# Optimization experiments

Hardware: AMD Instinct MI355X
Metric: run time of the kernel (lower is better)

The kernel has to match this reference:

```python
import jax, jax.numpy as jnp
import numpy as np

D_MODEL = 256
N_HEADS = 8
HEAD_DIM = D_MODEL // N_HEADS  # 32
N_LEVELS = 4
N_POINTS = 4
LEVEL_SHAPES = [(100, 100), (50, 50), (25, 25), (13, 13)]
LEVEL_STARTS = [0] + list(np.cumsum([h * w for h, w in LEVEL_SHAPES]))[:-1]
LEN_IN = int(sum(h * w for h, w in LEVEL_SHAPES))  # 13294
BATCH = 2
LEN_Q = LEN_IN  # encoder self-attention


def _offset_bias():
    # faithful to MSDeformAttn._reset_parameters for sampling_offsets bias
    thetas = np.arange(N_HEADS, dtype=np.float32) * (2.0 * np.pi / N_HEADS)
    grid = np.stack([np.cos(thetas), np.sin(thetas)], -1)
    grid = grid / np.abs(grid).max(-1, keepdims=True)
    grid = np.tile(grid.reshape(N_HEADS, 1, 1, 2), (1, N_LEVELS, N_POINTS, 1))
    for i in range(N_POINTS):
        grid[:, :, i, :] *= i + 1
    return jnp.asarray(grid.reshape(-1), dtype=jnp.float32)


def setup_inputs() -> dict:
    key = jax.random.key(0)
    ks = jax.random.split(key, 10)
    s = 1.0 / np.sqrt(D_MODEL)
    inp = {
        "query": jax.random.normal(ks[0], (BATCH, LEN_Q, D_MODEL), jnp.float32),
        "reference_points": jax.random.uniform(ks[1], (BATCH, LEN_Q, N_LEVELS, 2), jnp.float32),
        "input_flatten": jax.random.normal(ks[2], (BATCH, LEN_IN, D_MODEL), jnp.float32),
        "input_spatial_shapes": jnp.asarray(LEVEL_SHAPES, dtype=jnp.int32),
        "W_value": jax.random.normal(ks[3], (D_MODEL, D_MODEL), jnp.float32) * s,
        "b_value": jnp.zeros((D_MODEL,), jnp.float32),
        "W_off": jax.random.normal(ks[4], (D_MODEL, N_HEADS * N_LEVELS * N_POINTS * 2), jnp.float32) * 0.01,
        "b_off": _offset_bias(),
        "W_attn": jax.random.normal(ks[5], (D_MODEL, N_HEADS * N_LEVELS * N_POINTS), jnp.float32) * 0.01,
        "b_attn": jnp.zeros((N_HEADS * N_LEVELS * N_POINTS,), jnp.float32),
        "W_out": jax.random.normal(ks[6], (D_MODEL, D_MODEL), jnp.float32) * s,
        "b_out": jnp.zeros((D_MODEL,), jnp.float32),
    }
    return inp


def _corner(v_t, ix, iy, h, w):
    # v_t: (n, M, h*w, D); ix/iy: (n, M, LqP) int32. Zero padding outside.
    valid = (ix >= 0) & (ix < w) & (iy >= 0) & (iy < h)
    idx = jnp.clip(iy, 0, h - 1) * w + jnp.clip(ix, 0, w - 1)
    g = jnp.take_along_axis(v_t, idx[..., None], axis=2)  # (n, M, LqP, D)
    return g * valid[..., None].astype(v_t.dtype)


def _ms_deform_attn(query, reference_points, input_flatten,
                    W_value, b_value, W_off, b_off, W_attn, b_attn, W_out, b_out):
    n, lq, _ = query.shape
    value = (input_flatten @ W_value + b_value).reshape(n, LEN_IN, N_HEADS, HEAD_DIM)
    offs = (query @ W_off + b_off).reshape(n, lq, N_HEADS, N_LEVELS, N_POINTS, 2)
    aw = jax.nn.softmax(
        (query @ W_attn + b_attn).reshape(n, lq, N_HEADS, N_LEVELS * N_POINTS), axis=-1
    ).reshape(n, lq, N_HEADS, N_LEVELS, N_POINTS)
    # offset_normalizer = (w, h) per level
    norm = jnp.asarray([[w, h] for h, w in LEVEL_SHAPES], dtype=query.dtype)
    loc = reference_points[:, :, None, :, None, :] + offs / norm[None, None, None, :, None, :]

    acc = jnp.zeros((n, N_HEADS, lq, HEAD_DIM), dtype=value.dtype)
    for l, (h, w) in enumerate(LEVEL_SHAPES):
        s0 = LEVEL_STARTS[l]
        v_t = jnp.transpose(value[:, s0:s0 + h * w], (0, 2, 1, 3))  # (n, M, hw, D)
        ll = loc[:, :, :, l]  # (n, lq, M, P, 2) in [0,1]
        # grid_sample bilinear, align_corners=False: pixel = coord*size - 0.5
        x = ll[..., 0] * w - 0.5
        y = ll[..., 1] * h - 0.5
        x0 = jnp.floor(x); y0 = jnp.floor(y)
        tx = x - x0; ty = y - y0
        ix0 = x0.astype(jnp.int32); iy0 = y0.astype(jnp.int32)
        flat = lambda a: jnp.transpose(a, (0, 2, 1, 3)).reshape(n, N_HEADS, lq * N_POINTS)
        ix0f, iy0f = flat(ix0), flat(iy0)
        txf = flat(tx)[..., None]; tyf = flat(ty)[..., None]
        g00 = _corner(v_t, ix0f, iy0f, h, w)
        g01 = _corner(v_t, ix0f + 1, iy0f, h, w)
        g10 = _corner(v_t, ix0f, iy0f + 1, h, w)
        g11 = _corner(v_t, ix0f + 1, iy0f + 1, h, w)
        samp = (g00 * (1 - txf) * (1 - tyf) + g01 * txf * (1 - tyf)
                + g10 * (1 - txf) * tyf + g11 * txf * tyf)
        samp = samp.reshape(n, N_HEADS, lq, N_POINTS, HEAD_DIM)
        wl = jnp.transpose(aw[:, :, :, l], (0, 2, 1, 3))[..., None]  # (n, M, lq, P, 1)
        acc = acc + (samp * wl).sum(axis=3)

    out = jnp.transpose(acc, (0, 2, 1, 3)).reshape(n, lq, D_MODEL)
    return out @ W_out + b_out


def reference(query, reference_points, input_flatten, input_spatial_shapes,
              W_value, b_value, W_off, b_off, W_attn, b_attn, W_out, b_out):
    # input_spatial_shapes carried for signature fidelity; level geometry is static.
    return _ms_deform_attn(query, reference_points, input_flatten,
                           W_value, b_value, W_off, b_off, W_attn, b_attn, W_out, b_out)
```

## Files before the change

### kernel.cpp

```cpp
#include <hip/hip_runtime.h>

#define NH 8
#define HD 32
#define NL 4
#define NP 4
#define DM 256
#define LEN_IN_C 13294
#define LQ_C 13294
#define B_C 2
#define M_TOTAL (B_C * LQ_C)
#define MT_TILES 1662
#define RT32_TILES 831
#define GQ 32
#define QBLKS 831

typedef __attribute__((ext_vector_type(8))) short short8;
typedef __attribute__((ext_vector_type(4))) float floatx4;
typedef __attribute__((ext_vector_type(2))) float floatx2;

__device__ __forceinline__ unsigned short f2bf(float x) {
    union { float f; unsigned int u; } a; a.f = x;
    unsigned int r = (a.u + 0x7FFFu + ((a.u >> 16) & 1u)) >> 16;
    return (unsigned short)r;
}
__device__ __forceinline__ floatx2 up2(unsigned int u) {
    union { unsigned int u; float f; } lo, hi;
    lo.u = u << 16; hi.u = u & 0xffff0000u;
    floatx2 r; r.x = lo.f; r.y = hi.f; return r;
}
__device__ __forceinline__ unsigned int cvtpk_bf16(float lo, float hi) {
    unsigned int r;
    asm("v_cvt_pk_bf16_f32 %0, %1, %2" : "=v"(r) : "v"(lo), "v"(hi));
    return r;
}

__device__ __forceinline__ void conv_b_body(const float* __restrict__ W,
                                            unsigned short* __restrict__ Bsw,
                                            int Nsrc, int NTsrc, int NTtotal, int ntOff,
                                            int vblk) {
    const int u = vblk * 256 + threadIdx.x;
    const int lane = u & 63;
    const int unit = u >> 6;
    const int ntl = unit % NTsrc;
    const int kc = unit / NTsrc;
    const int n = ntl * 16 + (lane & 15);
    const int k0 = kc * 32 + (lane >> 4) * 8;
    short8 v;
#pragma unroll
    for (int j = 0; j < 8; ++j)
        v[j] = (short)f2bf(W[(size_t)(k0 + j) * Nsrc + n]);
    ((short8*)Bsw)[(size_t)(kc * NTtotal + ntOff + ntl) * 64 + lane] = v;
}

__global__ __launch_bounds__(256) void conv_weights_kernel(const float* __restrict__ Wv,
                                                           const float* __restrict__ Woff,
                                                           const float* __restrict__ Wattn,
                                                           const float* __restrict__ Wout,
                                                           const float* __restrict__ boff,
                                                           const float* __restrict__ battn,
                                                           unsigned short* __restrict__ BswV,
                                                           unsigned short* __restrict__ BswOA,
                                                           unsigned short* __restrict__ BswO,
                                                           float* __restrict__ fbias,
                                                           unsigned short* __restrict__ value,
                                                           unsigned short* __restrict__ AccSw) {
    const int blk = blockIdx.x;
    if (blk < 32)        conv_b_body(Wv,    BswV,  256, 16, 16, 0,  blk);
    else if (blk < 64)   conv_b_body(Woff,  BswOA, 256, 16, 24, 0,  blk - 32);
    else if (blk < 80)   conv_b_body(Wattn, BswOA, 128,  8, 24, 16, blk - 64);
    else if (blk < 112)  conv_b_body(Wout,  BswO,  256, 16, 16, 0,  blk - 80);
    else if (blk < 114) {
        const int t = (blk - 112) * 256 + threadIdx.x;
        if (t < 384) fbias[t] = (t < 256) ? boff[t] : battn[t - 256];
        else if (t < 416) {
            const int j = t - 384;
            value[-32 + j] = 0;
            value[(size_t)M_TOTAL * 256 + j] = 0;
        }
    } else {
        const int idx = threadIdx.x;
        if (idx < 128) {
            const int kc = idx >> 4;
            const int sub = idx & 15;
            const int lane = (12 + (sub & 3)) + 16 * (sub >> 2);
            const size_t unit = (size_t)(1661 * 8 + kc) * 64 + lane;
            short8 z = (short8){0, 0, 0, 0, 0, 0, 0, 0};
            ((short8*)AccSw)[unit] = z;
        }
    }
}

template <int NT, int OUTMODE>
__device__ __forceinline__ void gemm_lds_full(unsigned short* __restrict__ sA,
                                              const float* __restrict__ A,
                                              const unsigned short* __restrict__ Bsw,
                                              const float* __restrict__ bias,
                                              void* __restrict__ Cout, int M, int rt32) {
    constexpr int NTW = NT / 4;
    const int tid = threadIdx.x;
    const int lane = tid & 63;
    const int wave = tid >> 6;
    const int trow = rt32 * 32;

#pragma unroll
    for (int i = 0; i < 8; ++i) {
        const int li = i * 1024 + tid * 4;
        const int lrow = li >> 8;
        const int lcol = li & 255;
        const int srow = min(trow + lrow, M - 1);
        const float4 f = *(const float4*)(A + (size_t)srow * 256 + lcol);
        uint2 pk;
        pk.x = cvtpk_bf16(f.x, f.y);
        pk.y = cvtpk_bf16(f.z, f.w);
        const int lb = (li * 2) ^ ((lrow & 7) << 4);
        *(uint2*)((char*)sA + lb) = pk;
    }
    __syncthreads();

    const int m = lane & 15;
    const int q = lane >> 4;
    const short8* Bu = (const short8*)Bsw;

    floatx4 acc[2][NTW];
#pragma unroll
    for (int r = 0; r < 2; ++r)
#pragma unroll
        for (int t = 0; t < NTW; ++t) acc[r][t] = (floatx4){0.f, 0.f, 0.f, 0.f};

    const int swz = (m & 7) << 4;
#pragma unroll 2
    for (int kc = 0; kc < 8; ++kc) {
        const int fb0 = (m * 512 + kc * 64 + q * 16) ^ swz;
        const int fb1 = ((m + 16) * 512 + kc * 64 + q * 16) ^ swz;
        const short8 a0 = *(const short8*)((const char*)sA + fb0);
        const short8 a1 = *(const short8*)((const char*)sA + fb1);
#pragma unroll
        for (int t = 0; t < NTW; ++t) {
            const short8 b = Bu[(size_t)(kc * NT + wave * NTW + t) * 64 + lane];
            acc[0][t] = __builtin_amdgcn_mfma_f32_16x16x32_bf16(a0, b, acc[0][t], 0, 0, 0);
            acc[1][t] = __builtin_amdgcn_mfma_f32_16x16x32_bf16(a1, b, acc[1][t], 0, 0, 0);
        }
    }

    const int N = NT * 16;
    const int colq = lane & 15;
    const int rowq = (lane >> 4) * 4;
#pragma unroll
    for (int t = 0; t < NTW; ++t) {
        const int col = (wave * NTW + t) * 16 + colq;
        const float bc = bias[col];
#pragma unroll
        for (int r = 0; r < 2; ++r) {
#pragma unroll
            for (int reg = 0; reg < 4; ++reg) {
                const int row = trow + r * 16 + rowq + reg;
                if (row < M) {
                    const float v = acc[r][t][reg] + bc;
                    if (OUTMODE == 1) {
                        const int bb = row >= LEN_IN_C;
                        const int pos = row - (bb ? LEN_IN_C : 0);
                        const int hh = col >> 5;
                        const int dd = col & 31;
                        ((unsigned short*)Cout)[((size_t)((bb << 3) + hh) * LEN_IN_C + pos) * 32 + dd] = f2bf(v);
                    } else {
                        ((float*)Cout)[(size_t)row * N + col] = v;
                    }
                }
            }
        }
    }
}

__global__ __launch_bounds__(256) void front_gemm_kernel(const float* __restrict__ inflat,
                                                         const float* __restrict__ query,
                                                         const unsigned short* __restrict__ BswV,
                                                         const unsigned short* __restrict__ BswOA,
                                                         const float* __restrict__ bv,
                                                         const float* __restrict__ fbias,
                                                         unsigned short* __restrict__ value,
                                                         float* __restrict__ fused, int M) {
    __shared__ unsigned short sA[32 * 256];
    const int x = blockIdx.x;
    const int rt32 = x >> 1;
    if ((x & 1) == 0)
        gemm_lds_full<16, 1>(sA, inflat, BswV, bv, (void*)value, M, rt32);
    else
        gemm_lds_full<24, 0>(sA, query, BswOA, fbias, (void*)fused, M, rt32);
}

__global__ __launch_bounds__(256) void back_gemm_kernel(const unsigned short* __restrict__ Asw,
                                                        const unsigned short* __restrict__ Bsw,
                                                        const float* __restrict__ bias,
                                                        float* __restrict__ Cout, int M) {
    constexpr int NT = 16;
    constexpr int NTW = 4;
    const int tid = threadIdx.x;
    const int lane = tid & 63;
    const int wave = tid >> 6;
    const int rt = blockIdx.x;

    const short8* Au = (const short8*)Asw;
    const short8* Bu = (const short8*)Bsw;

    floatx4 acc[NTW];
#pragma unroll
    for (int t = 0; t < NTW; ++t) acc[t] = (floatx4){0.f, 0.f, 0.f, 0.f};

#pragma unroll 2
    for (int kc = 0; kc < 8; ++kc) {
        const short8 a = Au[(size_t)(rt * 8 + kc) * 64 + lane];
#pragma unroll
        for (int t = 0; t < NTW; ++t) {
            const short8 b = Bu[(size_t)(kc * NT + wave * NTW + t) * 64 + lane];
            acc[t] = __builtin_amdgcn_mfma_f32_16x16x32_bf16(a, b, acc[t], 0, 0, 0);
        }
    }

    const int colq = lane & 15;
    const int rowq = (lane >> 4) * 4;
#pragma unroll
    for (int t = 0; t < NTW; ++t) {
        const int col = (wave * NTW + t) * 16 + colq;
        const float bc = bias[col];
#pragma unroll
        for (int reg = 0; reg < 4; ++reg) {
            const int row = rt * 16 + rowq + reg;
            if (row < M)
                Cout[(size_t)row * 256 + col] = acc[t][reg] + bc;
        }
    }
}

__global__ __launch_bounds__(256, 8) void msda_sample_kernel(const float* __restrict__ refp,
                                                             const unsigned short* __restrict__ value,
                                                             const float* __restrict__ fused,
                                                             unsigned short* __restrict__ AccSw) {
    constexpr int lvl_hw[4] = {100, 50, 25, 13};
    constexpr int lvl_s[4] = {0, 10000, 12500, 13125};

    const int wg = blockIdx.x;
    const int h = wg & 7;
    const int q0 = (wg >> 3) * GQ;
    const int tid = threadIdx.x;

    __shared__ float s_ref[GQ * 8];
    __shared__ int2 s_pi[GQ * 17];
    __shared__ float4 s_pw[GQ * 17];

    s_ref[tid] = refp[min(q0 * 8 + tid, M_TOTAL * 8 - 1)];
    __syncthreads();

#pragma unroll
    for (int jj = 0; jj < 2; ++jj) {
        const int job = jj * 256 + tid;
        const int qq = job >> 4;
        const int t16 = job & 15;
        const int l = t16 >> 2;
        const int bq = min(q0 + qq, M_TOTAL - 1);
        const int b = (bq >= LQ_C) ? 1 : 0;

        const float logit = fused[(size_t)bq * 384 + 256 + h * 16 + t16];
        float m = logit;
#pragma unroll
        for (int mask = 1; mask < 16; mask <<= 1) m = fmaxf(m, __shfl_xor(m, mask));
        const float e = expf(logit - m);
        float s = e;
#pragma unroll
        for (int mask = 1; mask < 16; mask <<= 1) s += __shfl_xor(s, mask);
        const float aw = e / s;

        const int whl = lvl_hw[l];
        const float fwh = (float)whl;
        const float2 oxy = *(const float2*)(fused + (size_t)bq * 384 + (h * 16 + t16) * 2);
        const float x = s_ref[qq * 8 + l * 2] * fwh + oxy.x - 0.5f;
        const float y = s_ref[qq * 8 + l * 2 + 1] * fwh + oxy.y - 0.5f;
        const float x0f = floorf(x), y0f = floorf(y);
        const float tx = x - x0f, ty = y - y0f;
        const int ix0 = (int)x0f, iy0 = (int)y0f;

        const bool xv0 = (unsigned)ix0 < (unsigned)whl;
        const bool xv1 = (unsigned)(ix0 + 1) < (unsigned)whl;
        const bool yv0 = (unsigned)iy0 < (unsigned)whl;
        const bool yv1 = (unsigned)(iy0 + 1) < (unsigned)whl;

        const int cxp = min(max(ix0, -1), whl - 1);
        const int cy0 = min(max(iy0, 0), whl - 1);
        const int cy1 = min(max(iy0 + 1, 0), whl - 1);

        const int posb = (b * 8 + h) * LEN_IN_C + lvl_s[l];
        int2 aa;
        aa.x = (posb + cy0 * whl + cxp) * 64;
        aa.y = (posb + cy1 * whl + cxp) * 64;
        float4 wv;
        wv.x = (xv0 && yv0) ? aw * (1.f - tx) * (1.f - ty) : 0.f;
        wv.y = (xv1 && yv0) ? aw * tx * (1.f - ty) : 0.f;
        wv.z = (xv0 && yv1) ? aw * (1.f - tx) * ty : 0.f;
        wv.w = (xv1 && yv1) ? aw * tx * ty : 0.f;
        const int slot = qq * 17 + t16;
        s_pi[slot] = aa;
        s_pw[slot] = wv;
    }
    __syncthreads();

    const int qq = tid >> 3;
    const int l8 = tid & 7;
    const char* vbp = (const char*)value + l8 * 16;
    const int pbase = qq * 17;
    const bool right = (l8 & 4) != 0;

    floatx2 acc0 = (floatx2){0.f, 0.f}, acc1 = acc0, acc2 = acc0, acc3 = acc0;
#pragma unroll 2
    for (int pt = 0; pt < 16; ++pt) {
        const int2 aa = s_pi[pbase + pt];
        const float4 wv = s_pw[pbase + pt];
        const float wt = right ? wv.y : wv.x;
        const float wb = right ? wv.w : wv.z;
        const uint4 vt = *(const uint4*)(vbp + aa.x);
        const uint4 vbm = *(const uint4*)(vbp + aa.y);
        const floatx2 w2t = (floatx2){wt, wt};
        const floatx2 w2b = (floatx2){wb, wb};
        acc0 += w2t * up2(vt.x);
        acc1 += w2t * up2(vt.y);
        acc2 += w2t * up2(vt.z);
        acc3 += w2t * up2(vt.w);
        acc0 += w2b * up2(vbm.x);
        acc1 += w2b * up2(vbm.y);
        acc2 += w2b * up2(vbm.z);
        acc3 += w2b * up2(vbm.w);
    }

    float r0 = acc0.x, r1 = acc0.y, r2 = acc1.x, r3 = acc1.y;
    float r4 = acc2.x, r5 = acc2.y, r6 = acc3.x, r7 = acc3.y;
    r0 += __shfl_xor(r0, 4); r1 += __shfl_xor(r1, 4);
    r2 += __shfl_xor(r2, 4); r3 += __shfl_xor(r3, 4);
    r4 += __shfl_xor(r4, 4); r5 += __shfl_xor(r5, 4);
    r6 += __shfl_xor(r6, 4); r7 += __shfl_xor(r7, 4);

    const int bq = q0 + qq;
    if (!right && bq < M_TOTAL) {
        const int rt = bq >> 4, mm = bq & 15;
        const int unit = (rt * 8 + h) * 64 + ((l8 & 3) * 16 + mm);
        uint4 o;
        o.x = cvtpk_bf16(r0, r1);
        o.y = cvtpk_bf16(r2, r3);
        o.z = cvtpk_bf16(r4, r5);
        o.w = cvtpk_bf16(r6, r7);
        *(uint4*)(AccSw + (size_t)unit * 8) = o;
    }
}

extern "C" void kernel_launch(void* const* d_in, const int* in_sizes, int n_in,
                              void* d_out, int out_size, void* d_ws, size_t ws_size,
                              hipStream_t stream) {
    const float* query  = (const float*)d_in[0];
    const float* refp   = (const float*)d_in[1];
    const float* inflat = (const float*)d_in[2];
    const float* Wv    = (const float*)d_in[4];
    const float* bv    = (const float*)d_in[5];
    const float* Woff  = (const float*)d_in[6];
    const float* boff  = (const float*)d_in[7];
    const float* Wattn = (const float*)d_in[8];
    const float* battn = (const float*)d_in[9];
    const float* Wout  = (const float*)d_in[10];
    const float* bout  = (const float*)d_in[11];
    float* out = (float*)d_out;

    char* p = (char*)d_ws;
    unsigned short* AccSw = (unsigned short*)p;
    p += (size_t)MT_TILES * 8 * 64 * 8 * sizeof(unsigned short);
    unsigned short* BswV = (unsigned short*)p;   p += (size_t)8 * 16 * 64 * 8 * 2;
    unsigned short* BswOA = (unsigned short*)p;  p += (size_t)8 * 24 * 64 * 8 * 2;
    unsigned short* BswO = (unsigned short*)p;   p += (size_t)8 * 16 * 64 * 8 * 2;
    float* fbias = (float*)p;                    p += 384 * sizeof(float);
    unsigned short* value = (unsigned short*)p + 32;
    p += ((size_t)M_TOTAL * 256 + 64) * sizeof(unsigned short);
    float* fused = (float*)p;                    p += (size_t)M_TOTAL * 384 * 4;

    const int M = M_TOTAL;

    conv_weights_kernel<<<115, 256, 0, stream>>>(Wv, Woff, Wattn, Wout, boff, battn,
                                                 BswV, BswOA, BswO, fbias, value, AccSw);
    front_gemm_kernel<<<RT32_TILES * 2, 256, 0, stream>>>(inflat, query, BswV, BswOA,
                                                          bv, fbias, value, fused, M);
    msda_sample_kernel<<<QBLKS * 8, 256, 0, stream>>>(refp, value, fused, AccSw);
    back_gemm_kernel<<<MT_TILES, 256, 0, stream>>>(AccSw, BswO, bout, out, M);
}
```

Before: 195.0 us.

## Store value as fp16 with fma_mix sampling and enlarge GEMM row tiles

```diff
diff --git a/kernel.cpp b/kernel.cpp
--- a/kernel.cpp
+++ b/kernel.cpp
@@ -11,28 +11,33 @@
 #define M_TOTAL (B_C * LQ_C)
 #define MT_TILES 1662
 #define RT32_TILES 831
+#define VB64 416
 #define GQ 32
 #define QBLKS 831
 
 typedef __attribute__((ext_vector_type(8))) short short8;
 typedef __attribute__((ext_vector_type(4))) float floatx4;
-typedef __attribute__((ext_vector_type(2))) float floatx2;
 
 __device__ __forceinline__ unsigned short f2bf(float x) {
     union { float f; unsigned int u; } a; a.f = x;
     unsigned int r = (a.u + 0x7FFFu + ((a.u >> 16) & 1u)) >> 16;
     return (unsigned short)r;
 }
-__device__ __forceinline__ floatx2 up2(unsigned int u) {
-    union { unsigned int u; float f; } lo, hi;
-    lo.u = u << 16; hi.u = u & 0xffff0000u;
-    floatx2 r; r.x = lo.f; r.y = hi.f; return r;
+__device__ __forceinline__ unsigned short f2h(float x) {
+    unsigned int r;
+    asm("v_cvt_f16_f32 %0, %1" : "=v"(r) : "v"(x));
+    return (unsigned short)r;
 }
 __device__ __forceinline__ unsigned int cvtpk_bf16(float lo, float hi) {
     unsigned int r;
     asm("v_cvt_pk_bf16_f32 %0, %1, %2" : "=v"(r) : "v"(lo), "v"(hi));
     return r;
 }
+
+#define FMAMIX_LO(acc, v, w) \
+    asm("v_fma_mix_f32 %0, %1, %2, %0 op_sel_hi:[1,0,0]" : "+v"(acc) : "v"(v), "v"(w))
+#define FMAMIX_HI(acc, v, w) \
+    asm("v_fma_mix_f32 %0, %1, %2, %0 op_sel:[1,0,0] op_sel_hi:[1,0,0]" : "+v"(acc) : "v"(v), "v"(w))
 
 __device__ __forceinline__ void conv_b_body(const float* __restrict__ W,
                                             unsigned short* __restrict__ Bsw,
@@ -90,20 +95,21 @@
     }
 }
 
-template <int NT, int OUTMODE>
+template <int NT, int OUTMODE, int RT>
 __device__ __forceinline__ void gemm_lds_full(unsigned short* __restrict__ sA,
                                               const float* __restrict__ A,
                                               const unsigned short* __restrict__ Bsw,
                                               const float* __restrict__ bias,
-                                              void* __restrict__ Cout, int M, int rt32) {
+                                              void* __restrict__ Cout, int M, int rtb) {
     constexpr int NTW = NT / 4;
+    constexpr int ROWS = RT * 16;
     const int tid = threadIdx.x;
     const int lane = tid & 63;
     const int wave = tid >> 6;
-    const int trow = rt32 * 32;
-
-#pragma unroll
-    for (int i = 0; i < 8; ++i) {
+    const int trow = rtb * ROWS;
+
+#pragma unroll
+    for (int i = 0; i < RT * 4; ++i) {
         const int li = i * 1024 + tid * 4;
         const int lrow = li >> 8;
         const int lcol = li & 255;
@@ -121,24 +127,27 @@
     const int q = lane >> 4;
     const short8* Bu = (const short8*)Bsw;
 
-    floatx4 acc[2][NTW];
-#pragma unroll
-    for (int r = 0; r < 2; ++r)
+    floatx4 acc[RT][NTW];
+#pragma unroll
+    for (int r = 0; r < RT; ++r)
 #pragma unroll
         for (int t = 0; t < NTW; ++t) acc[r][t] = (floatx4){0.f, 0.f, 0.f, 0.f};
 
     const int swz = (m & 7) << 4;
 #pragma unroll 2
     for (int kc = 0; kc < 8; ++kc) {
-        const int fb0 = (m * 512 + kc * 64 + q * 16) ^ swz;
-        const int fb1 = ((m + 16) * 512 + kc * 64 + q * 16) ^ swz;
-        const short8 a0 = *(const short8*)((const char*)sA + fb0);
-        const short8 a1 = *(const short8*)((const char*)sA + fb1);
+        short8 a[RT];
+#pragma unroll
+        for (int r = 0; r < RT; ++r) {
+            const int fb = ((m + r * 16) * 512 + kc * 64 + q * 16) ^ swz;
+            a[r] = *(const short8*)((const char*)sA + fb);
+        }
 #pragma unroll
         for (int t = 0; t < NTW; ++t) {
             const short8 b = Bu[(size_t)(kc * NT + wave * NTW + t) * 64 + lane];
-            acc[0][t] = __builtin_amdgcn_mfma_f32_16x16x32_bf16(a0, b, acc[0][t], 0, 0, 0);
-            acc[1][t] = __builtin_amdgcn_mfma_f32_16x16x32_bf16(a1, b, acc[1][t], 0, 0, 0);
+#pragma unroll
+            for (int r = 0; r < RT; ++r)
+                acc[r][t] = __builtin_amdgcn_mfma_f32_16x16x32_bf16(a[r], b, acc[r][t], 0, 0, 0);
         }
     }
 
@@ -150,7 +159,7 @@
         const int col = (wave * NTW + t) * 16 + colq;
         const float bc = bias[col];
 #pragma unroll
-        for (int r = 0; r < 2; ++r) {
+        for (int r = 0; r < RT; ++r) {
 #pragma unroll
             for (int reg = 0; reg < 4; ++reg) {
                 const int row = trow + r * 16 + rowq + reg;
@@ -161,7 +170,7 @@
                         const int pos = row - (bb ? LEN_IN_C : 0);
                         const int hh = col >> 5;
                         const int dd = col & 31;
-                        ((unsigned short*)Cout)[((size_t)((bb << 3) + hh) * LEN_IN_C + pos) * 32 + dd] = f2bf(v);
+                        ((unsigned short*)Cout)[((size_t)((bb << 3) + hh) * LEN_IN_C + pos) * 32 + dd] = f2h(v);
                     } else {
                         ((float*)Cout)[(size_t)row * N + col] = v;
                     }
@@ -179,13 +188,12 @@
                                                          const float* __restrict__ fbias,
                                                          unsigned short* __restrict__ value,
                                                          float* __restrict__ fused, int M) {
-    __shared__ unsigned short sA[32 * 256];
+    __shared__ unsigned short sA[64 * 256];
     const int x = blockIdx.x;
-    const int rt32 = x >> 1;
-    if ((x & 1) == 0)
-        gemm_lds_full<16, 1>(sA, inflat, BswV, bv, (void*)value, M, rt32);
+    if (x < VB64)
+        gemm_lds_full<16, 1, 4>(sA, inflat, BswV, bv, (void*)value, M, x);
     else
-        gemm_lds_full<24, 0>(sA, query, BswOA, fbias, (void*)fused, M, rt32);
+        gemm_lds_full<24, 0, 2>(sA, query, BswOA, fbias, (void*)fused, M, x - VB64);
 }
 
 __global__ __launch_bounds__(256) void back_gemm_kernel(const unsigned short* __restrict__ Asw,
@@ -197,22 +205,26 @@
     const int tid = threadIdx.x;
     const int lane = tid & 63;
     const int wave = tid >> 6;
-    const int rt = blockIdx.x;
+    const int rt0 = blockIdx.x * 2;
 
     const short8* Au = (const short8*)Asw;
     const short8* Bu = (const short8*)Bsw;
 
-    floatx4 acc[NTW];
-#pragma unroll
-    for (int t = 0; t < NTW; ++t) acc[t] = (floatx4){0.f, 0.f, 0.f, 0.f};
+    floatx4 acc[2][NTW];
+#pragma unroll
+    for (int r = 0; r < 2; ++r)
+#pragma unroll
+        for (int t = 0; t < NTW; ++t) acc[r][t] = (floatx4){0.f, 0.f, 0.f, 0.f};
 
 #pragma unroll 2
     for (int kc = 0; kc < 8; ++kc) {
-        const short8 a = Au[(size_t)(rt * 8 + kc) * 64 + lane];
+        const short8 a0 = Au[(size_t)(rt0 * 8 + kc) * 64 + lane];
+        const short8 a1 = Au[(size_t)((rt0 + 1) * 8 + kc) * 64 + lane];
 #pragma unroll
         for (int t = 0; t < NTW; ++t) {
             const short8 b = Bu[(size_t)(kc * NT + wave * NTW + t) * 64 + lane];
-            acc[t] = __builtin_amdgcn_mfma_f32_16x16x32_bf16(a, b, acc[t], 0, 0, 0);
+            acc[0][t] = __builtin_amdgcn_mfma_f32_16x16x32_bf16(a0, b, acc[0][t], 0, 0, 0);
+            acc[1][t] = __builtin_amdgcn_mfma_f32_16x16x32_bf16(a1, b, acc[1][t], 0, 0, 0);
         }
     }
 
@@ -223,10 +235,13 @@
         const int col = (wave * NTW + t) * 16 + colq;
         const float bc = bias[col];
 #pragma unroll
-        for (int reg = 0; reg < 4; ++reg) {
-            const int row = rt * 16 + rowq + reg;
-            if (row < M)
-                Cout[(size_t)row * 256 + col] = acc[t][reg] + bc;
+        for (int r = 0; r < 2; ++r) {
+#pragma unroll
+            for (int reg = 0; reg < 4; ++reg) {
+                const int row = (rt0 + r) * 16 + rowq + reg;
+                if (row < M)
+                    Cout[(size_t)row * 256 + col] = acc[r][t][reg] + bc;
+            }
         }
     }
 }
@@ -245,7 +260,7 @@
 
     __shared__ float s_ref[GQ * 8];
     __shared__ int2 s_pi[GQ * 17];
-    __shared__ float4 s_pw[GQ * 17];
+    __shared__ float2 s_pw2[2][GQ * 17];
 
     s_ref[tid] = refp[min(q0 * 8 + tid, M_TOTAL * 8 - 1)];
     __syncthreads();
@@ -291,14 +306,14 @@
         int2 aa;
         aa.x = (posb + cy0 * whl + cxp) * 64;
         aa.y = (posb + cy1 * whl + cxp) * 64;
-        float4 wv;
-        wv.x = (xv0 && yv0) ? aw * (1.f - tx) * (1.f - ty) : 0.f;
-        wv.y = (xv1 && yv0) ? aw * tx * (1.f - ty) : 0.f;
-        wv.z = (xv0 && yv1) ? aw * (1.f - tx) * ty : 0.f;
-        wv.w = (xv1 && yv1) ? aw * tx * ty : 0.f;
+        const float w00 = (xv0 && yv0) ? aw * (1.f - tx) * (1.f - ty) : 0.f;
+        const float w01 = (xv1 && yv0) ? aw * tx * (1.f - ty) : 0.f;
+        const float w10 = (xv0 && yv1) ? aw * (1.f - tx) * ty : 0.f;
+        const float w11 = (xv1 && yv1) ? aw * tx * ty : 0.f;
         const int slot = qq * 17 + t16;
         s_pi[slot] = aa;
-        s_pw[slot] = wv;
+        s_pw2[0][slot] = make_float2(w00, w10);
+        s_pw2[1][slot] = make_float2(w01, w11);
     }
     __syncthreads();
 
@@ -306,45 +321,40 @@
     const int l8 = tid & 7;
     const char* vbp = (const char*)value + l8 * 16;
     const int pbase = qq * 17;
-    const bool right = (l8 & 4) != 0;
-
-    floatx2 acc0 = (floatx2){0.f, 0.f}, acc1 = acc0, acc2 = acc0, acc3 = acc0;
+    const int side = (l8 >> 2) & 1;
+
+    float a0 = 0.f, a1 = 0.f, a2 = 0.f, a3 = 0.f;
+    float a4 = 0.f, a5 = 0.f, a6 = 0.f, a7 = 0.f;
 #pragma unroll 2
     for (int pt = 0; pt < 16; ++pt) {
         const int2 aa = s_pi[pbase + pt];
-        const float4 wv = s_pw[pbase + pt];
-        const float wt = right ? wv.y : wv.x;
-        const float wb = right ? wv.w : wv.z;
+        const float2 ww = s_pw2[side][pbase + pt];
         const uint4 vt = *(const uint4*)(vbp + aa.x);
-        const uint4 vbm = *(const uint4*)(vbp + aa.y);
-        const floatx2 w2t = (floatx2){wt, wt};
-        const floatx2 w2b = (floatx2){wb, wb};
-        acc0 += w2t * up2(vt.x);
-        acc1 += w2t * up2(vt.y);
-        acc2 += w2t * up2(vt.z);
-        acc3 += w2t * up2(vt.w);
-        acc0 += w2b * up2(vbm.x);
-        acc1 += w2b * up2(vbm.y);
-        acc2 += w2b * up2(vbm.z);
-        acc3 += w2b * up2(vbm.w);
-    }
-
-    float r0 = acc0.x, r1 = acc0.y, r2 = acc1.x, r3 = acc1.y;
-    float r4 = acc2.x, r5 = acc2.y, r6 = acc3.x, r7 = acc3.y;
-    r0 += __shfl_xor(r0, 4); r1 += __shfl_xor(r1, 4);
-    r2 += __shfl_xor(r2, 4); r3 += __shfl_xor(r3, 4);
-    r4 += __shfl_xor(r4, 4); r5 += __shfl_xor(r5, 4);
-    r6 += __shfl_xor(r6, 4); r7 += __shfl_xor(r7, 4);
+        const uint4 vb = *(const uint4*)(vbp + aa.y);
+        FMAMIX_LO(a0, vt.x, ww.x); FMAMIX_HI(a1, vt.x, ww.x);
+        FMAMIX_LO(a2, vt.y, ww.x); FMAMIX_HI(a3, vt.y, ww.x);
+        FMAMIX_LO(a4, vt.z, ww.x); FMAMIX_HI(a5, vt.z, ww.x);
+        FMAMIX_LO(a6, vt.w, ww.x); FMAMIX_HI(a7, vt.w, ww.x);
+        FMAMIX_LO(a0, vb.x, ww.y); FMAMIX_HI(a1, vb.x, ww.y);
+        FMAMIX_LO(a2, vb.y, ww.y); FMAMIX_HI(a3, vb.y, ww.y);
+        FMAMIX_LO(a4, vb.z, ww.y); FMAMIX_HI(a5, vb.z, ww.y);
+        FMAMIX_LO(a6, vb.w, ww.y); FMAMIX_HI(a7, vb.w, ww.y);
+    }
+
+    a0 += __shfl_xor(a0, 4); a1 += __shfl_xor(a1, 4);
+    a2 += __shfl_xor(a2, 4); a3 += __shfl_xor(a3, 4);
+    a4 += __shfl_xor(a4, 4); a5 += __shfl_xor(a5, 4);
+    a6 += __shfl_xor(a6, 4); a7 += __shfl_xor(a7, 4);
 
     const int bq = q0 + qq;
-    if (!right && bq < M_TOTAL) {
+    if (side == 0 && bq < M_TOTAL) {
         const int rt = bq >> 4, mm = bq & 15;
         const int unit = (rt * 8 + h) * 64 + ((l8 & 3) * 16 + mm);
         uint4 o;
-        o.x = cvtpk_bf16(r0, r1);
-        o.y = cvtpk_bf16(r2, r3);
-        o.z = cvtpk_bf16(r4, r5);
-        o.w = cvtpk_bf16(r6, r7);
+        o.x = cvtpk_bf16(a0, a1);
+        o.y = cvtpk_bf16(a2, a3);
+        o.z = cvtpk_bf16(a4, a5);
+        o.w = cvtpk_bf16(a6, a7);
         *(uint4*)(AccSw + (size_t)unit * 8) = o;
     }
 }
@@ -380,8 +390,8 @@
 
     conv_weights_kernel<<<115, 256, 0, stream>>>(Wv, Woff, Wattn, Wout, boff, battn,
                                                  BswV, BswOA, BswO, fbias, value, AccSw);
-    front_gemm_kernel<<<RT32_TILES * 2, 256, 0, stream>>>(inflat, query, BswV, BswOA,
-                                                          bv, fbias, value, fused, M);
+    front_gemm_kernel<<<VB64 + RT32_TILES, 256, 0, stream>>>(inflat, query, BswV, BswOA,
+                                                             bv, fbias, value, fused, M);
     msda_sample_kernel<<<QBLKS * 8, 256, 0, stream>>>(refp, value, fused, AccSw);
-    back_gemm_kernel<<<MT_TILES, 256, 0, stream>>>(AccSw, BswO, bout, out, M);
-}
+    back_gemm_kernel<<<RT32_TILES, 256, 0, stream>>>(AccSw, BswO, bout, out, M);
+}
```

After: 193.4 us. About the same (-0.8%).
